# Kernel tuning notes

Measured on AMD Instinct MI355X. Metric: run time of the kernel, lower is better.

## Reference

```python
import jax, jax.numpy as jnp
import numpy as np

IN = 128          # in_channels
STEPS = 3         # processing_steps


def setup_inputs() -> dict:
    key = jax.random.key(0)
    ks = jax.random.split(key, 6)
    N, B = 500000, 1024
    x = jax.random.normal(ks[0], (N, IN), dtype=jnp.float32)
    batch = jnp.sort(jax.random.randint(ks[1], (N,), 0, B)).astype(jnp.int64)
    s = 1.0 / np.sqrt(IN)  # PyTorch LSTM init range
    w_ih = jax.random.uniform(ks[2], (4 * IN, 2 * IN), jnp.float32, -s, s)
    w_hh = jax.random.uniform(ks[3], (4 * IN, IN), jnp.float32, -s, s)
    b_ih = jax.random.uniform(ks[4], (4 * IN,), jnp.float32, -s, s)
    b_hh = jax.random.uniform(ks[5], (4 * IN,), jnp.float32, -s, s)
    return {"x": x, "w_ih": w_ih, "w_hh": w_hh, "b_ih": b_ih, "b_hh": b_hh,
            "batch": batch, "batch_size": B}


def reference(x, w_ih, w_hh, b_ih, b_hh, batch, batch_size):
    h = jnp.zeros((batch_size, IN), x.dtype)
    c = jnp.zeros((batch_size, IN), x.dtype)
    q_star = jnp.zeros((batch_size, 2 * IN), x.dtype)
    for _ in range(STEPS):
        # single-layer LSTM step (PyTorch gate order: i, f, g, o)
        gates = q_star @ w_ih.T + b_ih + h @ w_hh.T + b_hh
        i, f, g, o = jnp.split(gates, 4, axis=-1)
        c = jax.nn.sigmoid(f) * c + jax.nn.sigmoid(i) * jnp.tanh(g)
        h = jax.nn.sigmoid(o) * jnp.tanh(c)
        q = h  # [B, IN]
        # per-graph segment softmax over attention scores
        e = jnp.sum(x * q[batch], axis=-1)                       # [N]
        m = jax.ops.segment_max(e, batch, num_segments=batch_size)
        ex = jnp.exp(e - m[batch])
        denom = jax.ops.segment_sum(ex, batch, num_segments=batch_size)
        a = ex / denom[batch]                                    # [N]
        # weighted segment-sum readout
        r = jax.ops.segment_sum(x * a[:, None], batch, num_segments=batch_size)
        q_star = jnp.concatenate([q, r], axis=-1)                # [B, 2*IN]
    return q_star
```

## Files before the change

### kernel.cpp

```cpp
#include <hip/hip_runtime.h>
#include <math.h>

#define IN_CH 128
#define G4    512
#define K1    256
#define SPLIT 4

__device__ __forceinline__ float sigmoidf_(float v){ return 1.f/(1.f + expf(-v)); }

__device__ __forceinline__ float allreduce32_(float v){
  int t;
  t = __builtin_amdgcn_update_dpp(0, __float_as_int(v), 0xB1, 0xF, 0xF, true);
  v += __int_as_float(t);
  t = __builtin_amdgcn_update_dpp(0, __float_as_int(v), 0x4E, 0xF, 0xF, true);
  v += __int_as_float(t);
  t = __builtin_amdgcn_update_dpp(0, __float_as_int(v), 0x141, 0xF, 0xF, true);
  v += __int_as_float(t);
  t = __builtin_amdgcn_update_dpp(0, __float_as_int(v), 0x140, 0xF, 0xF, true);
  v += __int_as_float(t);
  t = __builtin_amdgcn_ds_swizzle(__float_as_int(v), 0x401F);
  return v + __int_as_float(t);
}

__global__ void transpose_w_kernel(const float* __restrict__ w_ih, const float* __restrict__ w_hh,
                                   float* __restrict__ wTih, float* __restrict__ wThh){
  int idx = blockIdx.x*blockDim.x + threadIdx.x;
  if (idx < G4*K1){ int g = idx / K1; int k = idx - g*K1; wTih[k*G4 + g] = w_ih[idx]; }
  if (idx < G4*IN_CH){ int g = idx / IN_CH; int k = idx - g*IN_CH; wThh[k*G4 + g] = w_hh[idx]; }
}

__global__ void seg_bounds_kernel(const int* __restrict__ batch, int N, int B, int* __restrict__ segs){
  int b = blockIdx.x*blockDim.x + threadIdx.x;
  if (b > B) return;
  if (b == B){ segs[B] = N; return; }
  int lo = 0, hi = N;
  while (lo < hi){ int mid = (lo + hi) >> 1; if (batch[mid] < b) lo = mid + 1; else hi = mid; }
  segs[b] = lo;
}

__global__ void lstm_init0_kernel(const float* __restrict__ b_ih, const float* __restrict__ b_hh,
                                  float* __restrict__ h, float* __restrict__ c,
                                  float* __restrict__ qstar, int B){
  int idx = blockIdx.x*blockDim.x + threadIdx.x;
  if (idx >= B*IN_CH) return;
  int b = idx >> 7, ch = idx & 127;
  float iv = sigmoidf_(b_ih[ch]          + b_hh[ch]);
  float gv = tanhf   (b_ih[2*IN_CH + ch] + b_hh[2*IN_CH + ch]);
  float ov = sigmoidf_(b_ih[3*IN_CH + ch] + b_hh[3*IN_CH + ch]);
  float cv = iv*gv;
  float hv = ov*tanhf(cv);
  c[idx] = cv; h[idx] = hv;
  qstar[b*K1 + ch] = hv;
}

__global__ __launch_bounds__(512) void lstm_fused_kernel(
    const float* __restrict__ qstar_in, float* __restrict__ h, float* __restrict__ c,
    const float* __restrict__ wTih, const float* __restrict__ wThh,
    const float* __restrict__ b_ih, const float* __restrict__ b_hh,
    float* __restrict__ qstar_out){
  int g    = threadIdx.x;
  int row0 = blockIdx.x*8;
  __shared__ float qs[8][K1];
  __shared__ float hs[8][IN_CH];
  __shared__ float gs[8][G4];
  for (int t = g; t < 8*K1; t += 512){ int r = t >> 8; int k = t & 255; qs[r][k] = qstar_in[(row0+r)*K1 + k]; }
  for (int t = g; t < 8*IN_CH; t += 512){ int r = t >> 7; int k = t & 127; hs[r][k] = h[(row0+r)*IN_CH + k]; }
  __syncthreads();
  float bias = b_ih[g] + b_hh[g];
  float acc[8];
#pragma unroll
  for (int r = 0; r < 8; ++r) acc[r] = bias;
  for (int k4 = 0; k4 < K1/4; ++k4){
    float w0 = wTih[(4*k4+0)*G4 + g];
    float w1 = wTih[(4*k4+1)*G4 + g];
    float w2 = wTih[(4*k4+2)*G4 + g];
    float w3 = wTih[(4*k4+3)*G4 + g];
#pragma unroll
    for (int r = 0; r < 8; ++r){
      float4 q = *reinterpret_cast<const float4*>(&qs[r][4*k4]);
      acc[r] += q.x*w0 + q.y*w1 + q.z*w2 + q.w*w3;
    }
  }
  for (int k4 = 0; k4 < IN_CH/4; ++k4){
    float w0 = wThh[(4*k4+0)*G4 + g];
    float w1 = wThh[(4*k4+1)*G4 + g];
    float w2 = wThh[(4*k4+2)*G4 + g];
    float w3 = wThh[(4*k4+3)*G4 + g];
#pragma unroll
    for (int r = 0; r < 8; ++r){
      float4 hv = *reinterpret_cast<const float4*>(&hs[r][4*k4]);
      acc[r] += hv.x*w0 + hv.y*w1 + hv.z*w2 + hv.w*w3;
    }
  }
#pragma unroll
  for (int r = 0; r < 8; ++r) gs[r][g] = acc[r];
  __syncthreads();
  for (int t = g; t < 8*IN_CH; t += 512){
    int r = t >> 7, ch = t & 127;
    int idx = (row0+r)*IN_CH + ch;
    float iv = sigmoidf_(gs[r][ch]);
    float fv = sigmoidf_(gs[r][IN_CH + ch]);
    float gv = tanhf(gs[r][2*IN_CH + ch]);
    float ov = sigmoidf_(gs[r][3*IN_CH + ch]);
    float cv = fv*c[idx] + iv*gv;
    float hv = ov*tanhf(cv);
    c[idx] = cv; h[idx] = hv;
    qstar_out[(row0+r)*K1 + ch] = hv;
  }
}

__global__ __launch_bounds__(256) void attn_part_kernel(const float* __restrict__ x,
    const float* __restrict__ qstar, const int* __restrict__ segs,
    float* __restrict__ pm, float* __restrict__ pd, float* __restrict__ pr){
  int b = blockIdx.x, p = blockIdx.y;
  int s = segs[b], t = segs[b+1];
  int len = t - s;
  int cs = s + (int)(((long long)len * p) / SPLIT);
  int ce = s + (int)(((long long)len * (p+1)) / SPLIT);
  int tid = threadIdx.x;
  int wave = tid >> 6, lane = tid & 63;
  int half = lane >> 5, lane31 = lane & 31;
  const float4* x4 = reinterpret_cast<const float4*>(x);
  float4 qv = *reinterpret_cast<const float4*>(&qstar[b*K1 + lane31*4]);

  float m = -INFINITY, d = 0.f;
  float rx = 0.f, ry = 0.f, rz = 0.f, rw = 0.f;
  const float4 z4 = make_float4(0.f,0.f,0.f,0.f);

  int stream = wave*2 + half;
  for (int j0 = cs + stream*2; j0 < ce; j0 += 16){
    int j1 = j0 + 1;
    bool v1 = (j1 < ce);
    float4 x0 = x4[(size_t)j0*(IN_CH/4) + lane31];
    float4 x1 = v1 ? x4[(size_t)j1*(IN_CH/4) + lane31] : z4;
    float e0 = x0.x*qv.x + x0.y*qv.y + x0.z*qv.z + x0.w*qv.w;
    float e1 = x1.x*qv.x + x1.y*qv.y + x1.z*qv.z + x1.w*qv.w;
    e0 = allreduce32_(e0);
    e1 = allreduce32_(e1);
    e1 = v1 ? e1 : -INFINITY;
    float em = fmaxf(e0, e1);
    if (em > m){
      float corr = __expf(m - em);
      d *= corr; rx *= corr; ry *= corr; rz *= corr; rw *= corr;
      m = em;
    }
    float p0 = __expf(e0 - m);
    float p1 = __expf(e1 - m);
    d += p0 + p1;
    rx += p0*x0.x + p1*x1.x;
    ry += p0*x0.y + p1*x1.y;
    rz += p0*x0.z + p1*x1.z;
    rw += p0*x0.w + p1*x1.w;
  }
  {
    float mo = __shfl_xor(m, 32);
    float dd = __shfl_xor(d, 32);
    float ox = __shfl_xor(rx, 32), oy = __shfl_xor(ry, 32);
    float oz = __shfl_xor(rz, 32), ow = __shfl_xor(rw, 32);
    float mn = fmaxf(m, mo);
    float c1 = (mn == -INFINITY) ? 0.f : __expf(m - mn);
    float c2 = (mn == -INFINITY) ? 0.f : __expf(mo - mn);
    d = d*c1 + dd*c2;
    rx = rx*c1 + ox*c2; ry = ry*c1 + oy*c2; rz = rz*c1 + oz*c2; rw = rw*c1 + ow*c2;
    m = mn;
  }
  __shared__ float mbuf[4], dbuf[4];
  __shared__ float rbuf[4][IN_CH];
  if (lane < 32){
    rbuf[wave][lane31*4+0] = rx; rbuf[wave][lane31*4+1] = ry;
    rbuf[wave][lane31*4+2] = rz; rbuf[wave][lane31*4+3] = rw;
  }
  if (lane == 0){ mbuf[wave] = m; dbuf[wave] = d; }
  __syncthreads();
  int part = b*SPLIT + p;
  if (tid < IN_CH){
    float M = fmaxf(fmaxf(mbuf[0], mbuf[1]), fmaxf(mbuf[2], mbuf[3]));
    float f0 = (M == -INFINITY) ? 0.f : __expf(mbuf[0] - M);
    float f1 = (M == -INFINITY) ? 0.f : __expf(mbuf[1] - M);
    float f2 = (M == -INFINITY) ? 0.f : __expf(mbuf[2] - M);
    float f3 = (M == -INFINITY) ? 0.f : __expf(mbuf[3] - M);
    float R = rbuf[0][tid]*f0 + rbuf[1][tid]*f1 + rbuf[2][tid]*f2 + rbuf[3][tid]*f3;
    pr[(size_t)part*IN_CH + tid] = R;
    if (tid == 0){
      pd[part] = dbuf[0]*f0 + dbuf[1]*f1 + dbuf[2]*f2 + dbuf[3]*f3;
      pm[part] = M;
    }
  }
}

__global__ void attn_combine_kernel(const float* __restrict__ pm, const float* __restrict__ pd,
                                    const float* __restrict__ pr, float* __restrict__ qstar){
  int b = blockIdx.x; int ch = threadIdx.x;
  float M = -INFINITY;
#pragma unroll
  for (int p = 0; p < SPLIT; ++p) M = fmaxf(M, pm[b*SPLIT + p]);
  float d = 0.f, r = 0.f;
#pragma unroll
  for (int p = 0; p < SPLIT; ++p){
    float mp = pm[b*SPLIT + p];
    float f = (mp == -INFINITY) ? 0.f : __expf(mp - M);
    d += pd[b*SPLIT + p] * f;
    r += pr[(size_t)(b*SPLIT + p)*IN_CH + ch] * f;
  }
  qstar[b*K1 + IN_CH + ch] = (d > 0.f) ? r/d : 0.f;
}

extern "C" void kernel_launch(void* const* d_in, const int* in_sizes, int n_in,
                              void* d_out, int out_size, void* d_ws, size_t ws_size,
                              hipStream_t stream){
  const float* x     = (const float*)d_in[0];
  const float* w_ih  = (const float*)d_in[1];
  const float* w_hh  = (const float*)d_in[2];
  const float* b_ih  = (const float*)d_in[3];
  const float* b_hh  = (const float*)d_in[4];
  const int*   batch = (const int*)d_in[5];
  int N = in_sizes[0] / IN_CH;
  int B = out_size / K1;
  float* out = (float*)d_out;

  float* ws    = (float*)d_ws;
  float* h     = ws;
  float* c     = h + (size_t)B*IN_CH;
  float* wTih  = c + (size_t)B*IN_CH;
  float* wThh  = wTih + K1*G4;
  int*   segs  = (int*)(wThh + IN_CH*G4);
  float* pm    = (float*)(segs + (B + 2));
  float* pd    = pm + (size_t)B*SPLIT;
  float* pr    = pd + (size_t)B*SPLIT;

  transpose_w_kernel<<<(G4*K1 + 255)/256, 256, 0, stream>>>(w_ih, w_hh, wTih, wThh);
  seg_bounds_kernel<<<(B + 256)/256, 256, 0, stream>>>(batch, N, B, segs);
  lstm_init0_kernel<<<(B*IN_CH + 255)/256, 256, 0, stream>>>(b_ih, b_hh, h, c, out, B);

  for (int step = 0; step < 3; ++step){
    if (step > 0)
      lstm_fused_kernel<<<B/8, 512, 0, stream>>>(out, h, c, wTih, wThh, b_ih, b_hh, out);
    attn_part_kernel<<<dim3(B, SPLIT), 256, 0, stream>>>(x, out, segs, pm, pd, pr);
    attn_combine_kernel<<<B, IN_CH, 0, stream>>>(pm, pd, pr, out);
  }
}
```

Before: 211.2 us.

## Fuse prologue kernels, fold attention combine into LSTM, use 16-lane row streams

Merges the weight transpose, segment-bounds search and initial LSTM step into a single prologue launch. The per-step attention combine is folded into the next LSTM kernel's shared-memory load, so only the final combine remains as its own launch. The attention kernel now gives each 16-lane group a whole 128-float row (two float4 per lane), doubling the rows in flight per wave, which needs an extra cross-group merge of the online-softmax state. The intent is fewer launches and more memory-level parallelism in the bandwidth-bound pass over x, at the cost of more registers and reduction steps.

```diff
diff --git a/kernel.cpp b/kernel.cpp
--- a/kernel.cpp
+++ b/kernel.cpp
@@ -8,7 +8,11 @@
 
 __device__ __forceinline__ float sigmoidf_(float v){ return 1.f/(1.f + expf(-v)); }
 
-__device__ __forceinline__ float allreduce32_(float v){
+__device__ __forceinline__ float dot4_(float4 a, float4 b){
+  return a.x*b.x + a.y*b.y + a.z*b.z + a.w*b.w;
+}
+
+__device__ __forceinline__ float reduce16_(float v){
   int t;
   t = __builtin_amdgcn_update_dpp(0, __float_as_int(v), 0xB1, 0xF, 0xF, true);
   v += __int_as_float(t);
@@ -18,43 +22,47 @@
   v += __int_as_float(t);
   t = __builtin_amdgcn_update_dpp(0, __float_as_int(v), 0x140, 0xF, 0xF, true);
   v += __int_as_float(t);
-  t = __builtin_amdgcn_ds_swizzle(__float_as_int(v), 0x401F);
-  return v + __int_as_float(t);
-}
-
-__global__ void transpose_w_kernel(const float* __restrict__ w_ih, const float* __restrict__ w_hh,
-                                   float* __restrict__ wTih, float* __restrict__ wThh){
-  int idx = blockIdx.x*blockDim.x + threadIdx.x;
-  if (idx < G4*K1){ int g = idx / K1; int k = idx - g*K1; wTih[k*G4 + g] = w_ih[idx]; }
-  if (idx < G4*IN_CH){ int g = idx / IN_CH; int k = idx - g*IN_CH; wThh[k*G4 + g] = w_hh[idx]; }
-}
-
-__global__ void seg_bounds_kernel(const int* __restrict__ batch, int N, int B, int* __restrict__ segs){
-  int b = blockIdx.x*blockDim.x + threadIdx.x;
-  if (b > B) return;
-  if (b == B){ segs[B] = N; return; }
-  int lo = 0, hi = N;
-  while (lo < hi){ int mid = (lo + hi) >> 1; if (batch[mid] < b) lo = mid + 1; else hi = mid; }
-  segs[b] = lo;
-}
-
-__global__ void lstm_init0_kernel(const float* __restrict__ b_ih, const float* __restrict__ b_hh,
-                                  float* __restrict__ h, float* __restrict__ c,
-                                  float* __restrict__ qstar, int B){
-  int idx = blockIdx.x*blockDim.x + threadIdx.x;
-  if (idx >= B*IN_CH) return;
-  int b = idx >> 7, ch = idx & 127;
-  float iv = sigmoidf_(b_ih[ch]          + b_hh[ch]);
-  float gv = tanhf   (b_ih[2*IN_CH + ch] + b_hh[2*IN_CH + ch]);
-  float ov = sigmoidf_(b_ih[3*IN_CH + ch] + b_hh[3*IN_CH + ch]);
-  float cv = iv*gv;
-  float hv = ov*tanhf(cv);
-  c[idx] = cv; h[idx] = hv;
-  qstar[b*K1 + ch] = hv;
+  return v;
+}
+
+__device__ __forceinline__ float swz16_(float v){
+  return __int_as_float(__builtin_amdgcn_ds_swizzle(__float_as_int(v), 0x401F));
+}
+
+__global__ void prologue_kernel(const float* __restrict__ w_ih, const float* __restrict__ w_hh,
+                                float* __restrict__ wTih, float* __restrict__ wThh,
+                                const int* __restrict__ batch, int N, int B, int* __restrict__ segs,
+                                const float* __restrict__ b_ih, const float* __restrict__ b_hh,
+                                float* __restrict__ h, float* __restrict__ c, float* __restrict__ qstar){
+  int blk = blockIdx.x;
+  if (blk < 512){
+    int idx = blk*256 + threadIdx.x;
+    { int g = idx / K1; int k = idx - g*K1; wTih[k*G4 + g] = w_ih[idx]; }
+    if (idx < G4*IN_CH){ int g = idx / IN_CH; int k = idx - g*IN_CH; wThh[k*G4 + g] = w_hh[idx]; }
+  } else if (blk < 517){
+    int b = (blk - 512)*256 + threadIdx.x;
+    if (b > B) return;
+    if (b == B){ segs[B] = N; return; }
+    int lo = 0, hi = N;
+    while (lo < hi){ int mid = (lo + hi) >> 1; if (batch[mid] < b) lo = mid + 1; else hi = mid; }
+    segs[b] = lo;
+  } else {
+    int idx = (blk - 517)*256 + threadIdx.x;
+    if (idx >= B*IN_CH) return;
+    int b = idx >> 7, ch = idx & 127;
+    float iv = sigmoidf_(b_ih[ch]           + b_hh[ch]);
+    float gv = tanhf    (b_ih[2*IN_CH + ch] + b_hh[2*IN_CH + ch]);
+    float ov = sigmoidf_(b_ih[3*IN_CH + ch] + b_hh[3*IN_CH + ch]);
+    float cv = iv*gv;
+    float hv = ov*tanhf(cv);
+    c[idx] = cv; h[idx] = hv;
+    qstar[b*K1 + ch] = hv;
+  }
 }
 
 __global__ __launch_bounds__(512) void lstm_fused_kernel(
-    const float* __restrict__ qstar_in, float* __restrict__ h, float* __restrict__ c,
+    const float* __restrict__ qstar, const float* __restrict__ pm, const float* __restrict__ pd,
+    const float* __restrict__ pr, float* __restrict__ h, float* __restrict__ c,
     const float* __restrict__ wTih, const float* __restrict__ wThh,
     const float* __restrict__ b_ih, const float* __restrict__ b_hh,
     float* __restrict__ qstar_out){
@@ -63,7 +71,20 @@
   __shared__ float qs[8][K1];
   __shared__ float hs[8][IN_CH];
   __shared__ float gs[8][G4];
-  for (int t = g; t < 8*K1; t += 512){ int r = t >> 8; int k = t & 255; qs[r][k] = qstar_in[(row0+r)*K1 + k]; }
+  for (int t = g; t < 8*IN_CH; t += 512){ int r = t >> 7; int k = t & 127; qs[r][k] = qstar[(row0+r)*K1 + k]; }
+  for (int t = g; t < 8*IN_CH; t += 512){
+    int r = t >> 7, ch = t & 127; int b = row0 + r;
+    float m0 = pm[b*SPLIT+0], m1 = pm[b*SPLIT+1], m2 = pm[b*SPLIT+2], m3 = pm[b*SPLIT+3];
+    float M = fmaxf(fmaxf(m0, m1), fmaxf(m2, m3));
+    float f0 = (M == -INFINITY) ? 0.f : __expf(m0 - M);
+    float f1 = (M == -INFINITY) ? 0.f : __expf(m1 - M);
+    float f2 = (M == -INFINITY) ? 0.f : __expf(m2 - M);
+    float f3 = (M == -INFINITY) ? 0.f : __expf(m3 - M);
+    float dd = pd[b*SPLIT+0]*f0 + pd[b*SPLIT+1]*f1 + pd[b*SPLIT+2]*f2 + pd[b*SPLIT+3]*f3;
+    float rr = pr[(size_t)(b*SPLIT+0)*IN_CH + ch]*f0 + pr[(size_t)(b*SPLIT+1)*IN_CH + ch]*f1
+             + pr[(size_t)(b*SPLIT+2)*IN_CH + ch]*f2 + pr[(size_t)(b*SPLIT+3)*IN_CH + ch]*f3;
+    qs[r][IN_CH + ch] = (dd > 0.f) ? rr/dd : 0.f;
+  }
   for (int t = g; t < 8*IN_CH; t += 512){ int r = t >> 7; int k = t & 127; hs[r][k] = h[(row0+r)*IN_CH + k]; }
   __syncthreads();
   float bias = b_ih[g] + b_hh[g];
@@ -119,58 +140,83 @@
   int ce = s + (int)(((long long)len * (p+1)) / SPLIT);
   int tid = threadIdx.x;
   int wave = tid >> 6, lane = tid & 63;
-  int half = lane >> 5, lane31 = lane & 31;
+  int grp = (lane >> 4) & 3, l16 = lane & 15;
+  int sid = wave*4 + grp;
+  const float4 z4 = make_float4(0.f,0.f,0.f,0.f);
   const float4* x4 = reinterpret_cast<const float4*>(x);
-  float4 qv = *reinterpret_cast<const float4*>(&qstar[b*K1 + lane31*4]);
+  const float4* q4 = reinterpret_cast<const float4*>(&qstar[(size_t)b*K1]);
+  float4 qa = q4[l16], qb = q4[16 + l16];
 
   float m = -INFINITY, d = 0.f;
-  float rx = 0.f, ry = 0.f, rz = 0.f, rw = 0.f;
-  const float4 z4 = make_float4(0.f,0.f,0.f,0.f);
-
-  int stream = wave*2 + half;
-  for (int j0 = cs + stream*2; j0 < ce; j0 += 16){
+  float4 ra = z4, rb = z4;
+
+  for (int j0 = cs + sid*2; j0 < ce; j0 += 32){
     int j1 = j0 + 1;
-    bool v1 = (j1 < ce);
-    float4 x0 = x4[(size_t)j0*(IN_CH/4) + lane31];
-    float4 x1 = v1 ? x4[(size_t)j1*(IN_CH/4) + lane31] : z4;
-    float e0 = x0.x*qv.x + x0.y*qv.y + x0.z*qv.z + x0.w*qv.w;
-    float e1 = x1.x*qv.x + x1.y*qv.y + x1.z*qv.z + x1.w*qv.w;
-    e0 = allreduce32_(e0);
-    e1 = allreduce32_(e1);
-    e1 = v1 ? e1 : -INFINITY;
+    bool ok1 = (j1 < ce);
+    const float4* r0 = x4 + (size_t)j0*(IN_CH/4);
+    const float4* r1 = x4 + (size_t)j1*(IN_CH/4);
+    float4 a0 = r0[l16],        b0 = r0[16 + l16];
+    float4 a1 = ok1 ? r1[l16] : z4, b1 = ok1 ? r1[16 + l16] : z4;
+    float e0 = dot4_(a0, qa) + dot4_(b0, qb);
+    float e1 = dot4_(a1, qa) + dot4_(b1, qb);
+    e0 = reduce16_(e0);
+    e1 = reduce16_(e1);
+    e1 = ok1 ? e1 : -INFINITY;
     float em = fmaxf(e0, e1);
     if (em > m){
       float corr = __expf(m - em);
-      d *= corr; rx *= corr; ry *= corr; rz *= corr; rw *= corr;
+      d *= corr;
+      ra.x *= corr; ra.y *= corr; ra.z *= corr; ra.w *= corr;
+      rb.x *= corr; rb.y *= corr; rb.z *= corr; rb.w *= corr;
       m = em;
     }
     float p0 = __expf(e0 - m);
     float p1 = __expf(e1 - m);
     d += p0 + p1;
-    rx += p0*x0.x + p1*x1.x;
-    ry += p0*x0.y + p1*x1.y;
-    rz += p0*x0.z + p1*x1.z;
-    rw += p0*x0.w + p1*x1.w;
+    ra.x += p0*a0.x + p1*a1.x; ra.y += p0*a0.y + p1*a1.y;
+    ra.z += p0*a0.z + p1*a1.z; ra.w += p0*a0.w + p1*a1.w;
+    rb.x += p0*b0.x + p1*b1.x; rb.y += p0*b0.y + p1*b1.y;
+    rb.z += p0*b0.z + p1*b1.z; rb.w += p0*b0.w + p1*b1.w;
   }
   {
-    float mo = __shfl_xor(m, 32);
-    float dd = __shfl_xor(d, 32);
-    float ox = __shfl_xor(rx, 32), oy = __shfl_xor(ry, 32);
-    float oz = __shfl_xor(rz, 32), ow = __shfl_xor(rw, 32);
+    float mo = swz16_(m), dd = swz16_(d);
+    float4 rao, rbo;
+    rao.x = swz16_(ra.x); rao.y = swz16_(ra.y); rao.z = swz16_(ra.z); rao.w = swz16_(ra.w);
+    rbo.x = swz16_(rb.x); rbo.y = swz16_(rb.y); rbo.z = swz16_(rb.z); rbo.w = swz16_(rb.w);
     float mn = fmaxf(m, mo);
     float c1 = (mn == -INFINITY) ? 0.f : __expf(m - mn);
     float c2 = (mn == -INFINITY) ? 0.f : __expf(mo - mn);
     d = d*c1 + dd*c2;
-    rx = rx*c1 + ox*c2; ry = ry*c1 + oy*c2; rz = rz*c1 + oz*c2; rw = rw*c1 + ow*c2;
+    ra.x = ra.x*c1 + rao.x*c2; ra.y = ra.y*c1 + rao.y*c2;
+    ra.z = ra.z*c1 + rao.z*c2; ra.w = ra.w*c1 + rao.w*c2;
+    rb.x = rb.x*c1 + rbo.x*c2; rb.y = rb.y*c1 + rbo.y*c2;
+    rb.z = rb.z*c1 + rbo.z*c2; rb.w = rb.w*c1 + rbo.w*c2;
     m = mn;
   }
+  {
+    float mo = __shfl_xor(m, 32), dd = __shfl_xor(d, 32);
+    float4 rao, rbo;
+    rao.x = __shfl_xor(ra.x, 32); rao.y = __shfl_xor(ra.y, 32);
+    rao.z = __shfl_xor(ra.z, 32); rao.w = __shfl_xor(ra.w, 32);
+    rbo.x = __shfl_xor(rb.x, 32); rbo.y = __shfl_xor(rb.y, 32);
+    rbo.z = __shfl_xor(rb.z, 32); rbo.w = __shfl_xor(rb.w, 32);
+    float mn = fmaxf(m, mo);
+    float c1 = (mn == -INFINITY) ? 0.f : __expf(m - mn);
+    float c2 = (mn == -INFINITY) ? 0.f : __expf(mo - mn);
+    d = d*c1 + dd*c2;
+    ra.x = ra.x*c1 + rao.x*c2; ra.y = ra.y*c1 + rao.y*c2;
+    ra.z = ra.z*c1 + rao.z*c2; ra.w = ra.w*c1 + rao.w*c2;
+    rb.x = rb.x*c1 + rbo.x*c2; rb.y = rb.y*c1 + rbo.y*c2;
+    rb.z = rb.z*c1 + rbo.z*c2; rb.w = rb.w*c1 + rbo.w*c2;
+    m = mn;
+  }
   __shared__ float mbuf[4], dbuf[4];
-  __shared__ float rbuf[4][IN_CH];
-  if (lane < 32){
-    rbuf[wave][lane31*4+0] = rx; rbuf[wave][lane31*4+1] = ry;
-    rbuf[wave][lane31*4+2] = rz; rbuf[wave][lane31*4+3] = rw;
-  }
-  if (lane == 0){ mbuf[wave] = m; dbuf[wave] = d; }
+  __shared__ float rbA[4][64], rbB[4][64];
+  if (lane < 16){
+    *reinterpret_cast<float4*>(&rbA[wave][l16*4]) = ra;
+    *reinterpret_cast<float4*>(&rbB[wave][l16*4]) = rb;
+    if (l16 == 0){ mbuf[wave] = m; dbuf[wave] = d; }
+  }
   __syncthreads();
   int part = b*SPLIT + p;
   if (tid < IN_CH){
@@ -179,8 +225,11 @@
     float f1 = (M == -INFINITY) ? 0.f : __expf(mbuf[1] - M);
     float f2 = (M == -INFINITY) ? 0.f : __expf(mbuf[2] - M);
     float f3 = (M == -INFINITY) ? 0.f : __expf(mbuf[3] - M);
-    float R = rbuf[0][tid]*f0 + rbuf[1][tid]*f1 + rbuf[2][tid]*f2 + rbuf[3][tid]*f3;
-    pr[(size_t)part*IN_CH + tid] = R;
+    float v0 = (tid < 64) ? rbA[0][tid] : rbB[0][tid-64];
+    float v1 = (tid < 64) ? rbA[1][tid] : rbB[1][tid-64];
+    float v2 = (tid < 64) ? rbA[2][tid] : rbB[2][tid-64];
+    float v3 = (tid < 64) ? rbA[3][tid] : rbB[3][tid-64];
+    pr[(size_t)part*IN_CH + tid] = v0*f0 + v1*f1 + v2*f2 + v3*f3;
     if (tid == 0){
       pd[part] = dbuf[0]*f0 + dbuf[1]*f1 + dbuf[2]*f2 + dbuf[3]*f3;
       pm[part] = M;
@@ -228,14 +277,13 @@
   float* pd    = pm + (size_t)B*SPLIT;
   float* pr    = pd + (size_t)B*SPLIT;
 
-  transpose_w_kernel<<<(G4*K1 + 255)/256, 256, 0, stream>>>(w_ih, w_hh, wTih, wThh);
-  seg_bounds_kernel<<<(B + 256)/256, 256, 0, stream>>>(batch, N, B, segs);
-  lstm_init0_kernel<<<(B*IN_CH + 255)/256, 256, 0, stream>>>(b_ih, b_hh, h, c, out, B);
-
-  for (int step = 0; step < 3; ++step){
-    if (step > 0)
-      lstm_fused_kernel<<<B/8, 512, 0, stream>>>(out, h, c, wTih, wThh, b_ih, b_hh, out);
+  prologue_kernel<<<517 + (B*IN_CH + 255)/256, 256, 0, stream>>>(
+      w_ih, w_hh, wTih, wThh, batch, N, B, segs, b_ih, b_hh, h, c, out);
+
+  attn_part_kernel<<<dim3(B, SPLIT), 256, 0, stream>>>(x, out, segs, pm, pd, pr);
+  for (int step = 1; step < 3; ++step){
+    lstm_fused_kernel<<<B/8, 512, 0, stream>>>(out, pm, pd, pr, h, c, wTih, wThh, b_ih, b_hh, out);
     attn_part_kernel<<<dim3(B, SPLIT), 256, 0, stream>>>(x, out, segs, pm, pd, pr);
-    attn_combine_kernel<<<B, IN_CH, 0, stream>>>(pm, pd, pr, out);
-  }
-}
+  }
+  attn_combine_kernel<<<B, IN_CH, 0, stream>>>(pm, pd, pr, out);
+}
```

Result: faster. 202.3 us (-4.3%).
